# Performance work log

Hardware: AMD Instinct MI355X
Metric: run time of the kernel (lower is better)

## Reference

```python
import jax, jax.numpy as jnp
import numpy as np

DIMS, K_SIZE, V_SIZE, SEQ_LEN = 1024, 128, 128, 2048
MINUS = -100.0


def setup_inputs() -> dict:
    key = jax.random.key(0)
    k1, k2, k3, k4, k5 = jax.random.split(key, 5)
    B, S = 8, 2048
    minibatch = jax.random.normal(k1, (B, S, DIMS), dtype=jnp.float32)
    # Linear params (torch nn.Linear default init scale ~ U(-1/sqrt(fan_in), ...)); use scaled normals
    s = 1.0 / np.sqrt(DIMS)
    Wk = jax.random.normal(k2, (DIMS, K_SIZE), dtype=jnp.float32) * s
    bk = jax.random.normal(k3, (K_SIZE,), dtype=jnp.float32) * s
    Wv = jax.random.normal(k4, (DIMS, V_SIZE), dtype=jnp.float32) * s
    bv = jax.random.normal(k5, (V_SIZE,), dtype=jnp.float32) * s
    return {"minibatch": minibatch, "Wk": Wk, "bk": bk, "Wv": Wv, "bv": bv,
            "current_seq_len": S}


def reference(minibatch, Wk, bk, Wv, bv, current_seq_len):
    # keys == queries (shared projection, as in the original forward)
    keys = minibatch @ Wk + bk              # [B,S,K]
    values = minibatch @ Wv + bv            # [B,S,V]
    S = current_seq_len
    mask = jnp.tril(jnp.ones((S, S), dtype=jnp.float32))  # [S,S] lower-triangular
    scores = jnp.einsum('bsk,btk->bst', keys, keys) / np.sqrt(K_SIZE)
    logits = mask * scores + MINUS * (1.0 - mask)
    probs = jax.nn.softmax(logits, axis=2)
    read = jnp.einsum('bst,btv->bsv', probs, values)  # [B,S,V]
    return jnp.concatenate([minibatch, read], axis=2)  # [B,S,dims+V]
```

## Files before the change

### kernel.cpp

```cpp
#include <hip/hip_runtime.h>
#include <hip/hip_bf16.h>

#define BATCH 8
#define SEQ   2048
#define DMS   1024
#define KSZ   128
#define OD    1152

typedef unsigned short u16;
typedef unsigned int   u32;
typedef __attribute__((ext_vector_type(4)))  float  f32x4;
typedef __attribute__((ext_vector_type(16))) float  f32x16;
typedef __attribute__((ext_vector_type(8)))  __bf16 bf16x8;

union U128 { uint4 u4; bf16x8 b8; u16 us[8]; u32 u[4]; };

__device__ inline u16 f2bf(float f) {
  union { __bf16 h; u16 u; } c;
  c.h = (__bf16)f;
  return c.u;
}

__device__ inline float fexp2(float x) {
  float r;
  asm("v_exp_f32 %0, %1" : "=v"(r) : "v"(x));
  return r;
}

__device__ inline f32x4 mfma16(bf16x8 a, bf16x8 b, f32x4 c) {
  return __builtin_amdgcn_mfma_f32_16x16x32_bf16(a, b, c, 0, 0, 0);
}
__device__ inline f32x16 mfma32(bf16x8 a, bf16x8 b, f32x16 c) {
  return __builtin_amdgcn_mfma_f32_32x32x16_bf16(a, b, c, 0, 0, 0);
}

__device__ inline uint4 pack8bf(float4 a, float4 b) {
  U128 w;
  w.us[0] = f2bf(a.x); w.us[1] = f2bf(a.y);
  w.us[2] = f2bf(a.z); w.us[3] = f2bf(a.w);
  w.us[4] = f2bf(b.x); w.us[5] = f2bf(b.y);
  w.us[6] = f2bf(b.z); w.us[7] = f2bf(b.w);
  return w.u4;
}

__device__ inline void glds16(const u16* src, u16* ldsDst) {
  __builtin_amdgcn_global_load_lds(
      (const __attribute__((address_space(1))) u32*)src,
      (__attribute__((address_space(3))) u32*)ldsDst, 16, 0, 0);
}

#define BSTRIDE 262144

__global__ void __launch_bounds__(256) prep_kernel(
    const float* __restrict__ Wk, const float* __restrict__ Wv,
    u16* __restrict__ Wtiles)
{
  int T = blockIdx.x * 256 + threadIdx.x;
  int n  = T & 255;
  int kc = (T >> 8) * 8;
  int ks = kc >> 6;
  int kk = kc & 63;
  const float* src = (n < 128) ? (Wk + n) : (Wv + (n - 128));
  U128 w;
#pragma unroll
  for (int j = 0; j < 8; ++j) w.us[j] = f2bf(src[(size_t)(kc + j) * KSZ]);
  u16* dst = Wtiles + ks * 16384 + n * 64 + (kk ^ ((n & 7) << 3));
  *(uint4*)dst = w.u4;
}

__global__ void __launch_bounds__(512, 1) proj_kernel(
    const float* __restrict__ X, const u16* __restrict__ Wtiles,
    const float* __restrict__ bk, const float* __restrict__ bv,
    float* __restrict__ out, u16* __restrict__ Kfrag, u16* __restrict__ Vfrag)
{
  __shared__ u16 Ab[2][64 * 64];
  __shared__ u16 Bt[2][256 * 64];

  const int tid  = threadIdx.x;
  const int lane = tid & 63;
  const int wv   = tid >> 6;
  const int wm   = wv >> 2;
  const int wn   = wv & 3;
  const int l15  = lane & 15;
  const int g    = lane >> 4;
  const int m0   = blockIdx.x * 64;

  const int ar = tid >> 3;
  const int ac = (tid & 7) * 8;

  const float* xrow = X + (size_t)(m0 + ar) * DMS + ac;
  float*       orow = out + (size_t)(m0 + ar) * OD + ac;
  const int   abOff = (ar * 128 + ac * 2) ^ ((ar & 7) << 4);

  char* AbB = (char*)&Ab[0][0];
  char* BtB = (char*)&Bt[0][0];

  f32x4 acc[2][4];
#pragma unroll
  for (int i = 0; i < 2; ++i)
#pragma unroll
    for (int j = 0; j < 4; ++j) acc[i][j] = (f32x4){0.f, 0.f, 0.f, 0.f};

  float4 xv[2][2];

  xv[0][0] = *(const float4*)(xrow);
  xv[0][1] = *(const float4*)(xrow + 4);
  {
    const u16* ws = Wtiles + wv * 512 + lane * 8;
    u16* wd = &Bt[0][0] + wv * 512;
#pragma unroll
    for (int r = 0; r < 4; ++r) glds16(ws + r * 4096, wd + r * 4096);
  }
  *(uint4*)(AbB + abOff) = pack8bf(xv[0][0], xv[0][1]);
  __syncthreads();

#pragma unroll
  for (int k = 0; k < 16; ++k) {
    const int cur = k & 1, nxt = cur ^ 1;
    *(float4*)(orow + k * 64)     = xv[cur][0];
    *(float4*)(orow + k * 64 + 4) = xv[cur][1];
    if (k < 15) {
      xv[nxt][0] = *(const float4*)(xrow + (k + 1) * 64);
      xv[nxt][1] = *(const float4*)(xrow + (k + 1) * 64 + 4);
      const u16* ws = Wtiles + (size_t)(k + 1) * 16384 + wv * 512 + lane * 8;
      u16* wd = &Bt[nxt][0] + wv * 512;
#pragma unroll
      for (int r = 0; r < 4; ++r) glds16(ws + r * 4096, wd + r * 4096);
    }
#pragma unroll
    for (int kh = 0; kh < 2; ++kh) {
      bf16x8 af[2], bfr[4];
#pragma unroll
      for (int mf = 0; mf < 2; ++mf) {
        int m = wm * 32 + mf * 16 + l15;
        int ab = cur * 8192 + ((m * 128 + (kh * 32 + g * 8) * 2) ^ ((m & 7) << 4));
        U128 u; u.u4 = *(uint4*)(AbB + ab); af[mf] = u.b8;
      }
#pragma unroll
      for (int nf = 0; nf < 4; ++nf) {
        int n = wn * 64 + nf * 16 + l15;
        int bb = cur * 32768 + ((n * 128 + (kh * 32 + g * 8) * 2) ^ ((n & 7) << 4));
        U128 u; u.u4 = *(uint4*)(BtB + bb); bfr[nf] = u.b8;
      }
#pragma unroll
      for (int mf = 0; mf < 2; ++mf)
#pragma unroll
        for (int nf = 0; nf < 4; ++nf)
          acc[mf][nf] = mfma16(af[mf], bfr[nf], acc[mf][nf]);
    }
    if (k < 15)
      *(uint4*)(AbB + nxt * 8192 + abOff) = pack8bf(xv[nxt][0], xv[nxt][1]);
    __syncthreads();
  }

  u16* Ct = &Bt[0][0];
#pragma unroll
  for (int nf = 0; nf < 4; ++nf) {
    int n = wn * 64 + nf * 16 + l15;
    float bias = (n < 128) ? bk[n] : bv[n - 128];
#pragma unroll
    for (int mf = 0; mf < 2; ++mf)
#pragma unroll
      for (int j = 0; j < 4; ++j) {
        int s = wm * 32 + mf * 16 + g * 4 + j;
        Ct[s * 256 + (n ^ ((s & 7) << 3))] = f2bf(acc[mf][nf][j] + bias);
      }
  }
  __syncthreads();

  const int bb    = m0 >> 11;
  const int tloc2 = (m0 & 2047) >> 5;

  {
    int sl = tid >> 3;
    int ks = tid & 7;
    int t2 = tloc2 + (sl >> 5);
    int lrow = sl & 31;
    u16* dst = Kfrag + (size_t)bb * BSTRIDE + (size_t)(t2 * 8 + ks) * 512 + lrow * 8;
#pragma unroll
    for (int hi2 = 0; hi2 < 2; ++hi2) {
      int n = ks * 16 + hi2 * 8;
      uint4 v = *(const uint4*)&Ct[sl * 256 + (n ^ ((sl & 7) << 3))];
      *(uint4*)(dst + hi2 * 256) = v;
    }
  }
  {
    int l31 = tid & 31;
    int vb2 = (tid >> 5) & 3;
    int thh = (tid >> 7) & 1;
    int sh2 = tid >> 8;
    int t2  = tloc2 + sh2;
    int n   = 128 + vb2 * 32 + l31;
    u16* dst = Vfrag + (size_t)bb * BSTRIDE +
               (size_t)((t2 * 4 + vb2) * 2 + thh) * 512 + l31 * 8;
#pragma unroll
    for (int hi = 0; hi < 2; ++hi) {
      U128 w;
#pragma unroll
      for (int j = 0; j < 8; ++j) {
        int s = sh2 * 32 + thh * 16 + hi * 8 + j;
        w.us[j] = Ct[s * 256 + (n ^ ((s & 7) << 3))];
      }
      *(uint4*)(dst + hi * 256) = w.u4;
    }
  }
}

__global__ void __launch_bounds__(256, 2) attn_kernel(
    const u16* __restrict__ Kfrag, const u16* __restrict__ Vfrag,
    float* __restrict__ out)
{
  __shared__ float Om[4][128][33];
  __shared__ float Ml[4][2][32];
  __shared__ float Wm[4][32];
  __shared__ float Li[32];

  const int tid  = threadIdx.x;
  const int lane = tid & 63;
  const int w    = tid >> 6;
  const int l31  = lane & 31;
  const int hi   = lane >> 5;

  const int bi = blockIdx.x;
  const int b  = bi & 7;
  const int qt = (bi < 256) ? (63 - (bi >> 3)) : ((bi >> 3) - 32);
  const int q0 = qt * 32;

  const u16* Kb = Kfrag + (size_t)b * BSTRIDE;
  const u16* Vb = Vfrag + (size_t)b * BSTRIDE;
  const int loff = hi * 256 + l31 * 8;

  bf16x8 qf[8];
  {
    const u16* qp = Kb + (size_t)(qt * 8) * 512 + loff;
#pragma unroll
    for (int ks = 0; ks < 8; ++ks) {
      U128 u; u.u4 = *(const uint4*)(qp + ks * 512); qf[ks] = u.b8;
    }
  }

  f32x16 o[4];
#pragma unroll
  for (int vb2 = 0; vb2 < 4; ++vb2)
#pragma unroll
    for (int i = 0; i < 16; ++i) o[vb2][i] = 0.f;

  float mrun = -3.0e38f, lsum = 0.f;
  const float SC  = 0.08838834764831845f;
  const float L2E = 1.44269504088896341f;

  bf16x8 kf[8];
  {
    int ti0 = (w <= qt) ? w : 0;
    const u16* kp = Kb + (size_t)(ti0 * 8) * 512 + loff;
#pragma unroll
    for (int ks = 0; ks < 8; ++ks) {
      U128 u; u.u4 = *(const uint4*)(kp + ks * 512); kf[ks] = u.b8;
    }
  }

  for (int ti = w; ti <= qt; ti += 4) {
    bf16x8 vf[4][2];
    {
      const u16* vp = Vb + (size_t)(ti * 8) * 512 + loff;
#pragma unroll
      for (int vb2 = 0; vb2 < 4; ++vb2)
#pragma unroll
        for (int th = 0; th < 2; ++th) {
          U128 u; u.u4 = *(const uint4*)(vp + (vb2 * 2 + th) * 512);
          vf[vb2][th] = u.b8;
        }
    }
    f32x16 s;
#pragma unroll
    for (int i = 0; i < 16; ++i) s[i] = 0.f;
#pragma unroll
    for (int ks = 0; ks < 8; ++ks) s = mfma32(kf[ks], qf[ks], s);
    {
      int tin = (ti + 4 <= qt) ? ti + 4 : ti;
      const u16* kp = Kb + (size_t)(tin * 8) * 512 + loff;
#pragma unroll
      for (int ks = 0; ks < 8; ++ks) {
        U128 u; u.u4 = *(const uint4*)(kp + ks * 512); kf[ks] = u.b8;
      }
    }
    float sv[16];
#pragma unroll
    for (int r = 0; r < 16; ++r) sv[r] = s[r] * SC;
    if (ti == qt) {
#pragma unroll
      for (int r = 0; r < 16; ++r) {
        int toff = (r & 3) + 8 * (r >> 2) + 4 * hi;
        if (toff > l31) sv[r] = -3.0e38f;
      }
    }
    float mx = sv[0];
#pragma unroll
    for (int r = 1; r < 16; ++r) mx = fmaxf(mx, sv[r]);
    mx = fmaxf(mx, __shfl_xor(mx, 32));
    float p[16];
    float ps = 0.f;
    if (__all(mx - mrun <= 8.0f)) {
#pragma unroll
      for (int r = 0; r < 16; ++r) { p[r] = fexp2((sv[r] - mrun) * L2E); ps += p[r]; }
      ps += __shfl_xor(ps, 32);
      lsum += ps;
    } else {
      float mnew = fmaxf(mrun, mx);
      float al = fexp2((mrun - mnew) * L2E);
#pragma unroll
      for (int r = 0; r < 16; ++r) { p[r] = fexp2((sv[r] - mnew) * L2E); ps += p[r]; }
      ps += __shfl_xor(ps, 32);
      lsum = lsum * al + ps;
      mrun = mnew;
#pragma unroll
      for (int vb2 = 0; vb2 < 4; ++vb2)
#pragma unroll
        for (int i = 0; i < 16; ++i) o[vb2][i] *= al;
    }
    u32 c01 = (u32)f2bf(p[0])  | ((u32)f2bf(p[1])  << 16);
    u32 c23 = (u32)f2bf(p[2])  | ((u32)f2bf(p[3])  << 16);
    u32 c45 = (u32)f2bf(p[4])  | ((u32)f2bf(p[5])  << 16);
    u32 c67 = (u32)f2bf(p[6])  | ((u32)f2bf(p[7])  << 16);
    u32 c89 = (u32)f2bf(p[8])  | ((u32)f2bf(p[9])  << 16);
    u32 cAB = (u32)f2bf(p[10]) | ((u32)f2bf(p[11]) << 16);
    u32 cCD = (u32)f2bf(p[12]) | ((u32)f2bf(p[13]) << 16);
    u32 cEF = (u32)f2bf(p[14]) | ((u32)f2bf(p[15]) << 16);
    u32 d01 = __shfl_xor(c01, 32);
    u32 d23 = __shfl_xor(c23, 32);
    u32 d45 = __shfl_xor(c45, 32);
    u32 d67 = __shfl_xor(c67, 32);
    u32 d89 = __shfl_xor(c89, 32);
    u32 dAB = __shfl_xor(cAB, 32);
    u32 dCD = __shfl_xor(cCD, 32);
    u32 dEF = __shfl_xor(cEF, 32);
    U128 pf1, pf2;
    pf1.u[0] = hi ? d45 : c01;
    pf1.u[1] = hi ? d67 : c23;
    pf1.u[2] = hi ? c45 : d01;
    pf1.u[3] = hi ? c67 : d23;
    pf2.u[0] = hi ? dCD : c89;
    pf2.u[1] = hi ? dEF : cAB;
    pf2.u[2] = hi ? cCD : d89;
    pf2.u[3] = hi ? cEF : dAB;
#pragma unroll
    for (int vb2 = 0; vb2 < 4; ++vb2) {
      o[vb2] = mfma32(vf[vb2][0], pf1.b8, o[vb2]);
      o[vb2] = mfma32(vf[vb2][1], pf2.b8, o[vb2]);
    }
  }

#pragma unroll
  for (int vb2 = 0; vb2 < 4; ++vb2)
#pragma unroll
    for (int r = 0; r < 16; ++r) {
      int v = vb2 * 32 + (r & 3) + 8 * (r >> 2) + 4 * hi;
      Om[w][v][l31] = o[vb2][r];
    }
  if (lane < 32) {
    Ml[w][0][l31] = mrun;
    Ml[w][1][l31] = lsum;
  }
  __syncthreads();

  if (tid < 32) {
    float m0 = Ml[0][0][tid], m1 = Ml[1][0][tid];
    float m2 = Ml[2][0][tid], m3 = Ml[3][0][tid];
    float M  = fmaxf(fmaxf(m0, m1), fmaxf(m2, m3));
    float w0 = fexp2((m0 - M) * L2E), w1 = fexp2((m1 - M) * L2E);
    float w2 = fexp2((m2 - M) * L2E), w3 = fexp2((m3 - M) * L2E);
    float L  = Ml[0][1][tid] * w0 + Ml[1][1][tid] * w1 +
               Ml[2][1][tid] * w2 + Ml[3][1][tid] * w3;
    Wm[0][tid] = w0; Wm[1][tid] = w1; Wm[2][tid] = w2; Wm[3][tid] = w3;
    Li[tid] = 1.f / L;
  }
  __syncthreads();

  {
    const int q = tid >> 3;
    const int vbase = (tid & 7) * 16;
    float wq0 = Wm[0][q], wq1 = Wm[1][q], wq2 = Wm[2][q], wq3 = Wm[3][q];
    float li = Li[q];
    float* orow = out + (size_t)(b * SEQ + q0 + q) * OD + 1024 + vbase;
#pragma unroll
    for (int i = 0; i < 16; i += 4) {
      float4 res;
      res.x = (Om[0][vbase + i + 0][q] * wq0 + Om[1][vbase + i + 0][q] * wq1 +
               Om[2][vbase + i + 0][q] * wq2 + Om[3][vbase + i + 0][q] * wq3) * li;
      res.y = (Om[0][vbase + i + 1][q] * wq0 + Om[1][vbase + i + 1][q] * wq1 +
               Om[2][vbase + i + 1][q] * wq2 + Om[3][vbase + i + 1][q] * wq3) * li;
      res.z = (Om[0][vbase + i + 2][q] * wq0 + Om[1][vbase + i + 2][q] * wq1 +
               Om[2][vbase + i + 2][q] * wq2 + Om[3][vbase + i + 2][q] * wq3) * li;
      res.w = (Om[0][vbase + i + 3][q] * wq0 + Om[1][vbase + i + 3][q] * wq1 +
               Om[2][vbase + i + 3][q] * wq2 + Om[3][vbase + i + 3][q] * wq3) * li;
      *(float4*)(orow + i) = res;
    }
  }
}

extern "C" void kernel_launch(void* const* d_in, const int* in_sizes, int n_in,
                              void* d_out, int out_size, void* d_ws, size_t ws_size,
                              hipStream_t stream)
{
  const float* X  = (const float*)d_in[0];
  const float* Wk = (const float*)d_in[1];
  const float* bk = (const float*)d_in[2];
  const float* Wv = (const float*)d_in[3];
  const float* bv = (const float*)d_in[4];
  float* out = (float*)d_out;

  u16* Kfrag  = (u16*)d_ws;
  u16* Vfrag  = Kfrag + (size_t)BATCH * BSTRIDE;
  u16* Wtiles = Vfrag + (size_t)BATCH * BSTRIDE;

  prep_kernel<<<dim3(128), dim3(256), 0, stream>>>(Wk, Wv, Wtiles);
  proj_kernel<<<dim3(256), dim3(512), 0, stream>>>(X, Wtiles, bk, bv, out, Kfrag, Vfrag);
  attn_kernel<<<dim3(512), dim3(256), 0, stream>>>(Kfrag, Vfrag, out);
}
```

Baseline: 67.17 us.

## Move minibatch copy into attention kernel and halve projection tile rows

The fp32 copy of the minibatch into the output is moved from the projection kernel into the attention kernel. There it is interleaved with the KV loop, so the memory-bound copy overlaps with MFMA work, and any leftover chunks are finished after the loop. The projection kernel now uses 32-row tiles with 256 threads and two blocks per CU, giving 512 blocks instead of 256 for better occupancy. The cost is that each weight tile is reloaded by twice as many blocks, and the attention kernel's register and memory pressure goes up.

```diff
diff --git a/kernel.cpp b/kernel.cpp
--- a/kernel.cpp
+++ b/kernel.cpp
@@ -68,29 +68,26 @@
   *(uint4*)dst = w.u4;
 }
 
-__global__ void __launch_bounds__(512, 1) proj_kernel(
+__global__ void __launch_bounds__(256, 2) proj_kernel(
     const float* __restrict__ X, const u16* __restrict__ Wtiles,
     const float* __restrict__ bk, const float* __restrict__ bv,
-    float* __restrict__ out, u16* __restrict__ Kfrag, u16* __restrict__ Vfrag)
+    u16* __restrict__ Kfrag, u16* __restrict__ Vfrag)
 {
-  __shared__ u16 Ab[2][64 * 64];
+  __shared__ u16 Ab[2][32 * 64];
   __shared__ u16 Bt[2][256 * 64];
 
   const int tid  = threadIdx.x;
   const int lane = tid & 63;
-  const int wv   = tid >> 6;
-  const int wm   = wv >> 2;
-  const int wn   = wv & 3;
+  const int wid  = tid >> 6;
   const int l15  = lane & 15;
   const int g    = lane >> 4;
-  const int m0   = blockIdx.x * 64;
+  const int m0   = blockIdx.x * 32;
 
   const int ar = tid >> 3;
   const int ac = (tid & 7) * 8;
 
-  const float* xrow = X + (size_t)(m0 + ar) * DMS + ac;
-  float*       orow = out + (size_t)(m0 + ar) * OD + ac;
-  const int   abOff = (ar * 128 + ac * 2) ^ ((ar & 7) << 4);
+  const float* xrow  = X + (size_t)(m0 + ar) * DMS + ac;
+  const int    abOff = (ar * 128 + ac * 2) ^ ((ar & 7) << 4);
 
   char* AbB = (char*)&Ab[0][0];
   char* BtB = (char*)&Bt[0][0];
@@ -106,10 +103,10 @@
   xv[0][0] = *(const float4*)(xrow);
   xv[0][1] = *(const float4*)(xrow + 4);
   {
-    const u16* ws = Wtiles + wv * 512 + lane * 8;
-    u16* wd = &Bt[0][0] + wv * 512;
-#pragma unroll
-    for (int r = 0; r < 4; ++r) glds16(ws + r * 4096, wd + r * 4096);
+    const u16* ws = Wtiles + wid * 4096 + lane * 8;
+    u16* wd = &Bt[0][0] + wid * 4096;
+#pragma unroll
+    for (int r = 0; r < 8; ++r) glds16(ws + r * 512, wd + r * 512);
   }
   *(uint4*)(AbB + abOff) = pack8bf(xv[0][0], xv[0][1]);
   __syncthreads();
@@ -117,28 +114,26 @@
 #pragma unroll
   for (int k = 0; k < 16; ++k) {
     const int cur = k & 1, nxt = cur ^ 1;
-    *(float4*)(orow + k * 64)     = xv[cur][0];
-    *(float4*)(orow + k * 64 + 4) = xv[cur][1];
     if (k < 15) {
       xv[nxt][0] = *(const float4*)(xrow + (k + 1) * 64);
       xv[nxt][1] = *(const float4*)(xrow + (k + 1) * 64 + 4);
-      const u16* ws = Wtiles + (size_t)(k + 1) * 16384 + wv * 512 + lane * 8;
-      u16* wd = &Bt[nxt][0] + wv * 512;
-#pragma unroll
-      for (int r = 0; r < 4; ++r) glds16(ws + r * 4096, wd + r * 4096);
+      const u16* ws = Wtiles + (size_t)(k + 1) * 16384 + wid * 4096 + lane * 8;
+      u16* wd = &Bt[nxt][0] + wid * 4096;
+#pragma unroll
+      for (int r = 0; r < 8; ++r) glds16(ws + r * 512, wd + r * 512);
     }
 #pragma unroll
     for (int kh = 0; kh < 2; ++kh) {
       bf16x8 af[2], bfr[4];
 #pragma unroll
       for (int mf = 0; mf < 2; ++mf) {
-        int m = wm * 32 + mf * 16 + l15;
-        int ab = cur * 8192 + ((m * 128 + (kh * 32 + g * 8) * 2) ^ ((m & 7) << 4));
+        int m = mf * 16 + l15;
+        int ab = cur * 4096 + ((m * 128 + (kh * 32 + g * 8) * 2) ^ ((m & 7) << 4));
         U128 u; u.u4 = *(uint4*)(AbB + ab); af[mf] = u.b8;
       }
 #pragma unroll
       for (int nf = 0; nf < 4; ++nf) {
-        int n = wn * 64 + nf * 16 + l15;
+        int n = wid * 64 + nf * 16 + l15;
         int bb = cur * 32768 + ((n * 128 + (kh * 32 + g * 8) * 2) ^ ((n & 7) << 4));
         U128 u; u.u4 = *(uint4*)(BtB + bb); bfr[nf] = u.b8;
       }
@@ -149,34 +144,32 @@
           acc[mf][nf] = mfma16(af[mf], bfr[nf], acc[mf][nf]);
     }
     if (k < 15)
-      *(uint4*)(AbB + nxt * 8192 + abOff) = pack8bf(xv[nxt][0], xv[nxt][1]);
+      *(uint4*)(AbB + nxt * 4096 + abOff) = pack8bf(xv[nxt][0], xv[nxt][1]);
     __syncthreads();
   }
 
   u16* Ct = &Bt[0][0];
 #pragma unroll
   for (int nf = 0; nf < 4; ++nf) {
-    int n = wn * 64 + nf * 16 + l15;
+    int n = wid * 64 + nf * 16 + l15;
     float bias = (n < 128) ? bk[n] : bv[n - 128];
 #pragma unroll
     for (int mf = 0; mf < 2; ++mf)
 #pragma unroll
       for (int j = 0; j < 4; ++j) {
-        int s = wm * 32 + mf * 16 + g * 4 + j;
+        int s = mf * 16 + g * 4 + j;
         Ct[s * 256 + (n ^ ((s & 7) << 3))] = f2bf(acc[mf][nf][j] + bias);
       }
   }
   __syncthreads();
 
-  const int bb    = m0 >> 11;
-  const int tloc2 = (m0 & 2047) >> 5;
+  const int bb   = m0 >> 11;
+  const int tloc = (m0 & 2047) >> 5;
 
   {
     int sl = tid >> 3;
     int ks = tid & 7;
-    int t2 = tloc2 + (sl >> 5);
-    int lrow = sl & 31;
-    u16* dst = Kfrag + (size_t)bb * BSTRIDE + (size_t)(t2 * 8 + ks) * 512 + lrow * 8;
+    u16* dst = Kfrag + (size_t)bb * BSTRIDE + (size_t)(tloc * 8 + ks) * 512 + sl * 8;
 #pragma unroll
     for (int hi2 = 0; hi2 < 2; ++hi2) {
       int n = ks * 16 + hi2 * 8;
@@ -187,18 +180,16 @@
   {
     int l31 = tid & 31;
     int vb2 = (tid >> 5) & 3;
-    int thh = (tid >> 7) & 1;
-    int sh2 = tid >> 8;
-    int t2  = tloc2 + sh2;
+    int th  = tid >> 7;
     int n   = 128 + vb2 * 32 + l31;
     u16* dst = Vfrag + (size_t)bb * BSTRIDE +
-               (size_t)((t2 * 4 + vb2) * 2 + thh) * 512 + l31 * 8;
+               (size_t)((tloc * 4 + vb2) * 2 + th) * 512 + l31 * 8;
 #pragma unroll
     for (int hi = 0; hi < 2; ++hi) {
       U128 w;
 #pragma unroll
       for (int j = 0; j < 8; ++j) {
-        int s = sh2 * 32 + thh * 16 + hi * 8 + j;
+        int s = th * 16 + hi * 8 + j;
         w.us[j] = Ct[s * 256 + (n ^ ((s & 7) << 3))];
       }
       *(uint4*)(dst + hi * 256) = w.u4;
@@ -208,7 +199,7 @@
 
 __global__ void __launch_bounds__(256, 2) attn_kernel(
     const u16* __restrict__ Kfrag, const u16* __restrict__ Vfrag,
-    float* __restrict__ out)
+    const float* __restrict__ X, float* __restrict__ out)
 {
   __shared__ float Om[4][128][33];
   __shared__ float Ml[4][2][32];
@@ -230,6 +221,12 @@
   const u16* Vb = Vfrag + (size_t)b * BSTRIDE;
   const int loff = hi * 256 + l31 * 8;
 
+  const int cr = tid >> 3;
+  const int cs = (tid & 7) * 32;
+  const float4* csrc = (const float4*)(X + (size_t)(b * SEQ + q0 + cr) * DMS) + cs;
+  float4*       cdst = (float4*)(out + (size_t)(b * SEQ + q0 + cr) * OD) + cs;
+  int cidx = 0;
+
   bf16x8 qf[8];
   {
     const u16* qp = Kb + (size_t)(qt * 8) * 512 + loff;
@@ -270,6 +267,11 @@
           U128 u; u.u4 = *(const uint4*)(vp + (vb2 * 2 + th) * 512);
           vf[vb2][th] = u.b8;
         }
+    }
+    if (cidx < 32) {
+      float4 t0 = csrc[cidx], t1 = csrc[cidx + 1];
+      cdst[cidx] = t0; cdst[cidx + 1] = t1;
+      cidx += 2;
     }
     f32x16 s;
 #pragma unroll
@@ -350,6 +352,13 @@
     }
   }
 
+  for (; cidx < 32; cidx += 4) {
+    float4 t0 = csrc[cidx], t1 = csrc[cidx + 1];
+    float4 t2 = csrc[cidx + 2], t3 = csrc[cidx + 3];
+    cdst[cidx] = t0; cdst[cidx + 1] = t1;
+    cdst[cidx + 2] = t2; cdst[cidx + 3] = t3;
+  }
+
 #pragma unroll
   for (int vb2 = 0; vb2 < 4; ++vb2)
 #pragma unroll
@@ -414,6 +423,6 @@
   u16* Wtiles = Vfrag + (size_t)BATCH * BSTRIDE;
 
   prep_kernel<<<dim3(128), dim3(256), 0, stream>>>(Wk, Wv, Wtiles);
-  proj_kernel<<<dim3(256), dim3(512), 0, stream>>>(X, Wtiles, bk, bv, out, Kfrag, Vfrag);
-  attn_kernel<<<dim3(512), dim3(256), 0, stream>>>(Kfrag, Vfrag, out);
-}
+  proj_kernel<<<dim3(512), dim3(256), 0, stream>>>(X, Wtiles, bk, bv, Kfrag, Vfrag);
+  attn_kernel<<<dim3(512), dim3(256), 0, stream>>>(Kfrag, Vfrag, X, out);
+}
```

Result: slower. 100.1 us (+49.1%).
